# Kernel tuning notes

Measured on AMD Instinct MI355X. Metric: run time of the kernel, lower is better.

## Reference

```python
import jax, jax.numpy as jnp
import numpy as np

EMBED_DIM = 512
EDGE_COUNT = 200
BATCH = 1024
N_SBJ = 1      # subject entities per example
N_OBJ = 64     # candidate object entities per example


def setup_inputs() -> dict:
    key = jax.random.key(0)
    k1, k2, k3, k4 = jax.random.split(key, 4)
    sbj_embs = jax.random.normal(k1, (BATCH, N_SBJ, EMBED_DIM), dtype=jnp.float32)
    obj_embs = jax.random.normal(k2, (BATCH, N_OBJ, EMBED_DIM), dtype=jnp.float32)
    rel_ids = jax.random.randint(k3, (BATCH,), 0, EDGE_COUNT, dtype=jnp.int64)
    # W_r initialized as diagonal matrices from uniform values (as in __init__),
    # but stored as full dense [edge_count, d, d] trainable tensor.
    diag_vals = jax.random.uniform(k4, (EDGE_COUNT, EMBED_DIM), dtype=jnp.float32)
    W_r = jax.vmap(jnp.diag)(diag_vals)  # [edge_count, d, d]
    return {"sbj_embs": sbj_embs, "obj_embs": obj_embs, "rel_ids": rel_ids, "W_r": W_r}


def reference(sbj_embs, obj_embs, rel_ids, W_r):
    # rel_embs: gather per-relation dense matrix  [B, d, d]
    rel_embs = W_r[rel_ids]
    # sbj_rel = sbj @ rel : [B, n, d]
    sbj_rel = jnp.einsum('bnd,bde->bne', sbj_embs, rel_embs)
    # scores = sbj_rel @ obj^T : [B, n, m], then sum over n -> [B, m]
    scores = jnp.einsum('bne,bme->bm', sbj_rel, obj_embs)
    return scores
```

## Files before the change

### kernel.cpp

```cpp
#include <hip/hip_runtime.h>


#define D        512
#define NOBJ     64
#define EDGES    200
#define G        8
#define CSPL     4

__device__ __forceinline__ float4 f4zero() { float4 z; z.x=z.y=z.z=z.w=0.f; return z; }

__global__ __launch_bounds__(256) void prep_kernel(
    const int* __restrict__ rel, int B,
    int* __restrict__ sorted, int* __restrict__ chunk_rel,
    int* __restrict__ chunk_start, int* __restrict__ chunk_cnt,
    int* __restrict__ nchunks)
{
    __shared__ int cnt[EDGES];
    __shared__ int off[EDGES];
    __shared__ int pos[EDGES];
    __shared__ int nch;
    const int t = threadIdx.x;

    if (t < EDGES) cnt[t] = 0;
    if (t == 0) nch = 0;
    __syncthreads();

    for (int b = t; b < B; b += 256) atomicAdd(&cnt[rel[b]], 1);
    __syncthreads();

    if (t == 0) {
        int a = 0;
        for (int r = 0; r < EDGES; ++r) { off[r] = a; a += cnt[r]; }
    }
    if (t < EDGES) pos[t] = 0;
    __syncthreads();

    for (int b = t; b < B; b += 256) {
        const int r = rel[b];
        const int p = atomicAdd(&pos[r], 1);
        sorted[off[r] + p] = b;
    }

    if (t < EDGES) {
        const int n = cnt[t];
        if (n > 0) {
            const int nc   = (n + G - 1) / G;
            const int base = atomicAdd(&nch, nc);
            for (int k = 0; k < nc; ++k) {
                chunk_rel[base + k]   = t;
                chunk_start[base + k] = off[t] + k * G;
                chunk_cnt[base + k]   = min(G, n - k * G);
            }
        }
    }
    __syncthreads();
    if (t == 0) *nchunks = nch;
}

__global__ __launch_bounds__(256) void gemv_kernel(
    const float* __restrict__ sbj, const float* __restrict__ Wr,
    const int* __restrict__ sorted,
    const int* __restrict__ chunk_rel, const int* __restrict__ chunk_start,
    const int* __restrict__ chunk_cnt, const int* __restrict__ nchunks,
    float* __restrict__ V)
{
    const int cid = blockIdx.x >> 2;
    if (cid >= *nchunks) return;
    const int colbase = (blockIdx.x & 3) * 128;
    const int t    = threadIdx.x;
    const int lane = t & 31;
    const int rg   = t >> 5;

    __shared__ float lds[8192];

    const int relid = chunk_rel[cid];
    const int start = chunk_start[cid];
    const int cnt   = chunk_cnt[cid];

    #pragma unroll
    for (int g = 0; g < G; ++g) {
        float2 v2; v2.x = 0.f; v2.y = 0.f;
        if (g < cnt)
            v2 = reinterpret_cast<const float2*>(sbj + (size_t)sorted[start + g] * D)[t];
        lds[g * D + 2 * t]     = v2.x;
        lds[g * D + 2 * t + 1] = v2.y;
    }
    __syncthreads();

    const float4* __restrict__ W4 =
        reinterpret_cast<const float4*>(Wr) + (size_t)relid * (D * D / 4) + (colbase >> 2) + lane;

    float4 acc[G];
    #pragma unroll
    for (int g = 0; g < G; ++g) acc[g] = f4zero();

    #pragma unroll 8
    for (int d8 = 0; d8 < D; d8 += 8) {
        const int row = d8 + rg;
        const float4 w = W4[(size_t)row * (D / 4)];
        #pragma unroll
        for (int g = 0; g < G; ++g) {
            const float sg = lds[g * D + row];
            acc[g].x = fmaf(sg, w.x, acc[g].x);
            acc[g].y = fmaf(sg, w.y, acc[g].y);
            acc[g].z = fmaf(sg, w.z, acc[g].z);
            acc[g].w = fmaf(sg, w.w, acc[g].w);
        }
    }
    __syncthreads();

    #pragma unroll
    for (int g = 0; g < G; ++g)
        reinterpret_cast<float4*>(lds)[(rg * G + g) * 32 + lane] = acc[g];
    __syncthreads();

    const int col = t & 127;
    const int gg  = t >> 7;
    #pragma unroll
    for (int gi = 0; gi < 4; ++gi) {
        const int g = gg * 4 + gi;
        if (g < cnt) {
            float s = 0.f;
            #pragma unroll
            for (int r = 0; r < 8; ++r) s += lds[(r * G + g) * 128 + col];
            V[(size_t)sorted[start + g] * D + colbase + col] = s;
        }
    }
}

__global__ __launch_bounds__(256) void score_kernel(
    const float* __restrict__ V, const float* __restrict__ obj,
    float* __restrict__ out)
{
    const int b    = blockIdx.x;
    const int t    = threadIdx.x;
    const int lane = t & 63;
    const int wv   = t >> 6;

    const float4* __restrict__ v4 = reinterpret_cast<const float4*>(V + (size_t)b * D);
    const float4 a = v4[lane * 2];
    const float4 c = v4[lane * 2 + 1];
    float vreg[8] = {a.x, a.y, a.z, a.w, c.x, c.y, c.z, c.w};

    const float* __restrict__ objb = obj + (size_t)b * NOBJ * D;

    #pragma unroll 4
    for (int j = 0; j < 16; ++j) {
        const int m = wv * 16 + j;
        const float4* __restrict__ o4 = reinterpret_cast<const float4*>(objb + (size_t)m * D);
        const float4 x = o4[lane * 2];
        const float4 y = o4[lane * 2 + 1];

        float p = vreg[0] * x.x + vreg[1] * x.y + vreg[2] * x.z + vreg[3] * x.w
                + vreg[4] * y.x + vreg[5] * y.y + vreg[6] * y.z + vreg[7] * y.w;

        #pragma unroll
        for (int off = 32; off > 0; off >>= 1)
            p += __shfl_down(p, off, 64);

        if (lane == 0) out[(size_t)b * NOBJ + m] = p;
    }
}

__global__ __launch_bounds__(256) void fused_kernel(
    const float* __restrict__ sbj, const float* __restrict__ obj,
    const int* __restrict__ rel, const float* __restrict__ Wr,
    float* __restrict__ out)
{
    const int b = blockIdx.x;
    const int t = threadIdx.x;
    __shared__ float s_lds[D];
    __shared__ float v_lds[D];
    {
        const float2 sv = reinterpret_cast<const float2*>(sbj + (size_t)b * D)[t];
        s_lds[2 * t] = sv.x; s_lds[2 * t + 1] = sv.y;
    }
    __syncthreads();
    const float2* __restrict__ W2 = reinterpret_cast<const float2*>(Wr + (size_t)rel[b] * D * D);
    float acc0 = 0.f, acc1 = 0.f;
    #pragma unroll 8
    for (int d = 0; d < D; ++d) {
        const float sd = s_lds[d];
        const float2 w = W2[d * (D / 2) + t];
        acc0 = fmaf(sd, w.x, acc0); acc1 = fmaf(sd, w.y, acc1);
    }
    v_lds[2 * t] = acc0; v_lds[2 * t + 1] = acc1;
    __syncthreads();
    const int wave = t >> 6, lane = t & 63;
    float vreg[8];
    #pragma unroll
    for (int k = 0; k < 8; ++k) vreg[k] = v_lds[lane * 8 + k];
    const float* __restrict__ objb = obj + (size_t)b * NOBJ * D;
    #pragma unroll 4
    for (int j = 0; j < 16; ++j) {
        const int m = wave * 16 + j;
        const float4* __restrict__ o4 = reinterpret_cast<const float4*>(objb + (size_t)m * D);
        const float4 a = o4[lane * 2];
        const float4 c = o4[lane * 2 + 1];
        float p = vreg[0]*a.x + vreg[1]*a.y + vreg[2]*a.z + vreg[3]*a.w
                + vreg[4]*c.x + vreg[5]*c.y + vreg[6]*c.z + vreg[7]*c.w;
        #pragma unroll
        for (int off = 32; off > 0; off >>= 1) p += __shfl_down(p, off, 64);
        if (lane == 0) out[(size_t)b * NOBJ + m] = p;
    }
}

extern "C" void kernel_launch(void* const* d_in, const int* in_sizes, int n_in,
                              void* d_out, int out_size, void* d_ws, size_t ws_size,
                              hipStream_t stream) {
    const float* sbj = (const float*)d_in[0];
    const float* obj = (const float*)d_in[1];
    const int*   rel = (const int*)d_in[2];
    const float* Wr  = (const float*)d_in[3];
    float*       out = (float*)d_out;
    const int B = in_sizes[2];

    const int maxch = B / G + EDGES;

    const size_t offV      = 0;
    const size_t offSorted = (size_t)B * D * 4;
    const size_t offCRel   = offSorted + (size_t)B * 4;
    const size_t offCStart = offCRel   + (size_t)maxch * 4;
    const size_t offCCnt   = offCStart + (size_t)maxch * 4;
    const size_t offNCh    = offCCnt   + (size_t)maxch * 4;
    const size_t needed    = offNCh + 64;

    if (ws_size < needed) {
        fused_kernel<<<dim3(B), dim3(256), 0, stream>>>(sbj, obj, rel, Wr, out);
        return;
    }

    char* ws = (char*)d_ws;
    float* V           = (float*)(ws + offV);
    int*   sorted      = (int*)(ws + offSorted);
    int*   chunk_rel   = (int*)(ws + offCRel);
    int*   chunk_start = (int*)(ws + offCStart);
    int*   chunk_cnt   = (int*)(ws + offCCnt);
    int*   nchunks     = (int*)(ws + offNCh);

    prep_kernel<<<dim3(1), dim3(256), 0, stream>>>(rel, B, sorted, chunk_rel,
                                                   chunk_start, chunk_cnt, nchunks);
    gemv_kernel<<<dim3(CSPL * maxch), dim3(256), 0, stream>>>(sbj, Wr, sorted,
                                                              chunk_rel, chunk_start,
                                                              chunk_cnt, nchunks, V);
    score_kernel<<<dim3(B), dim3(256), 0, stream>>>(V, obj, out);
}
```

Measured before the change: 375.1 us.

## Fuse score computation into grouped GEMV kernel and parallelize prep scan

Removes the separate score kernel and the intermediate V buffer. Each GEMV block now dots its 128-column slice of the projected subject vector against the matching object columns and accumulates partial scores into the output with atomics. The output is zeroed with a memset first. The single-thread prefix sum in prep is also replaced by a parallel shared-memory scan. This saves the V write and read round trip and one launch, at the cost of four atomic adds per score and an extra memset.

```diff
diff --git a/kernel.cpp b/kernel.cpp
--- a/kernel.cpp
+++ b/kernel.cpp
@@ -15,24 +15,32 @@
     int* __restrict__ chunk_start, int* __restrict__ chunk_cnt,
     int* __restrict__ nchunks)
 {
-    __shared__ int cnt[EDGES];
-    __shared__ int off[EDGES];
-    __shared__ int pos[EDGES];
+    __shared__ int cnt[256];
+    __shared__ int scan[256];
+    __shared__ int off[256];
+    __shared__ int pos[256];
     __shared__ int nch;
     const int t = threadIdx.x;
 
-    if (t < EDGES) cnt[t] = 0;
+    cnt[t] = 0;
+    pos[t] = 0;
     if (t == 0) nch = 0;
     __syncthreads();
 
     for (int b = t; b < B; b += 256) atomicAdd(&cnt[rel[b]], 1);
     __syncthreads();
 
-    if (t == 0) {
-        int a = 0;
-        for (int r = 0; r < EDGES; ++r) { off[r] = a; a += cnt[r]; }
-    }
-    if (t < EDGES) pos[t] = 0;
+    int val = cnt[t];
+    scan[t] = val;
+    __syncthreads();
+    #pragma unroll
+    for (int o = 1; o < 256; o <<= 1) {
+        int v = (t >= o) ? scan[t - o] : 0;
+        __syncthreads();
+        scan[t] += v;
+        __syncthreads();
+    }
+    off[t] = scan[t] - val;
     __syncthreads();
 
     for (int b = t; b < B; b += 256) {
@@ -57,38 +65,45 @@
     if (t == 0) *nchunks = nch;
 }
 
-__global__ __launch_bounds__(256) void gemv_kernel(
-    const float* __restrict__ sbj, const float* __restrict__ Wr,
-    const int* __restrict__ sorted,
+__global__ __launch_bounds__(256) void main_kernel(
+    const float* __restrict__ sbj, const float* __restrict__ obj,
+    const float* __restrict__ Wr,  const int* __restrict__ sorted,
     const int* __restrict__ chunk_rel, const int* __restrict__ chunk_start,
     const int* __restrict__ chunk_cnt, const int* __restrict__ nchunks,
-    float* __restrict__ V)
+    float* __restrict__ out)
 {
     const int cid = blockIdx.x >> 2;
     if (cid >= *nchunks) return;
     const int colbase = (blockIdx.x & 3) * 128;
-    const int t    = threadIdx.x;
-    const int lane = t & 31;
-    const int rg   = t >> 5;
-
-    __shared__ float lds[8192];
+    const int t      = threadIdx.x;
+    const int lane32 = t & 31;
+    const int rg     = t >> 5;
+
+    __shared__ float lds[8192 + 1056];
+    float* s_s   = lds;
+    float* s_par = lds;
+    float* s_vs  = lds + 8192;
 
     const int relid = chunk_rel[cid];
     const int start = chunk_start[cid];
     const int cnt   = chunk_cnt[cid];
 
+    int bidx[G];
+    #pragma unroll
+    for (int g = 0; g < G; ++g) bidx[g] = (g < cnt) ? sorted[start + g] : -1;
+
     #pragma unroll
     for (int g = 0; g < G; ++g) {
         float2 v2; v2.x = 0.f; v2.y = 0.f;
         if (g < cnt)
-            v2 = reinterpret_cast<const float2*>(sbj + (size_t)sorted[start + g] * D)[t];
-        lds[g * D + 2 * t]     = v2.x;
-        lds[g * D + 2 * t + 1] = v2.y;
+            v2 = reinterpret_cast<const float2*>(sbj + (size_t)bidx[g] * D)[t];
+        s_s[g * D + 2 * t]     = v2.x;
+        s_s[g * D + 2 * t + 1] = v2.y;
     }
     __syncthreads();
 
     const float4* __restrict__ W4 =
-        reinterpret_cast<const float4*>(Wr) + (size_t)relid * (D * D / 4) + (colbase >> 2) + lane;
+        reinterpret_cast<const float4*>(Wr) + (size_t)relid * (D * D / 4) + (colbase >> 2) + lane32;
 
     float4 acc[G];
     #pragma unroll
@@ -100,7 +115,7 @@
         const float4 w = W4[(size_t)row * (D / 4)];
         #pragma unroll
         for (int g = 0; g < G; ++g) {
-            const float sg = lds[g * D + row];
+            const float sg = s_s[g * D + row];
             acc[g].x = fmaf(sg, w.x, acc[g].x);
             acc[g].y = fmaf(sg, w.y, acc[g].y);
             acc[g].z = fmaf(sg, w.z, acc[g].z);
@@ -111,54 +126,41 @@
 
     #pragma unroll
     for (int g = 0; g < G; ++g)
-        reinterpret_cast<float4*>(lds)[(rg * G + g) * 32 + lane] = acc[g];
-    __syncthreads();
-
-    const int col = t & 127;
-    const int gg  = t >> 7;
-    #pragma unroll
-    for (int gi = 0; gi < 4; ++gi) {
-        const int g = gg * 4 + gi;
-        if (g < cnt) {
+        reinterpret_cast<float4*>(s_par)[(rg * G + g) * 32 + lane32] = acc[g];
+    __syncthreads();
+
+    {
+        const int col = t & 127;
+        const int gg  = t >> 7;
+        #pragma unroll
+        for (int gi = 0; gi < 4; ++gi) {
+            const int g = gg * 4 + gi;
             float s = 0.f;
             #pragma unroll
-            for (int r = 0; r < 8; ++r) s += lds[(r * G + g) * 128 + col];
-            V[(size_t)sorted[start + g] * D + colbase + col] = s;
-        }
-    }
-}
-
-__global__ __launch_bounds__(256) void score_kernel(
-    const float* __restrict__ V, const float* __restrict__ obj,
-    float* __restrict__ out)
-{
-    const int b    = blockIdx.x;
-    const int t    = threadIdx.x;
-    const int lane = t & 63;
-    const int wv   = t >> 6;
-
-    const float4* __restrict__ v4 = reinterpret_cast<const float4*>(V + (size_t)b * D);
-    const float4 a = v4[lane * 2];
-    const float4 c = v4[lane * 2 + 1];
-    float vreg[8] = {a.x, a.y, a.z, a.w, c.x, c.y, c.z, c.w};
-
-    const float* __restrict__ objb = obj + (size_t)b * NOBJ * D;
-
-    #pragma unroll 4
-    for (int j = 0; j < 16; ++j) {
-        const int m = wv * 16 + j;
-        const float4* __restrict__ o4 = reinterpret_cast<const float4*>(objb + (size_t)m * D);
-        const float4 x = o4[lane * 2];
-        const float4 y = o4[lane * 2 + 1];
-
-        float p = vreg[0] * x.x + vreg[1] * x.y + vreg[2] * x.z + vreg[3] * x.w
-                + vreg[4] * y.x + vreg[5] * y.y + vreg[6] * y.z + vreg[7] * y.w;
-
-        #pragma unroll
-        for (int off = 32; off > 0; off >>= 1)
-            p += __shfl_down(p, off, 64);
-
-        if (lane == 0) out[(size_t)b * NOBJ + m] = p;
+            for (int r = 0; r < 8; ++r) s += s_par[(r * G + g) * 128 + col];
+            s_vs[g * 132 + (col >> 5) * 33 + (col & 31)] = s;
+        }
+    }
+    __syncthreads();
+
+    const int pair = t & 3;
+    const int m    = t >> 2;
+
+    for (int g = 0; g < cnt; ++g) {
+        const float* __restrict__ op =
+            obj + (size_t)bidx[g] * NOBJ * D + (size_t)m * D + colbase + pair * 32;
+        const float* __restrict__ vp = s_vs + g * 132 + pair * 33;
+
+        float p = 0.f;
+        #pragma unroll
+        for (int j = 0; j < 8; ++j) {
+            const float4 o = reinterpret_cast<const float4*>(op)[j];
+            p += vp[4 * j]     * o.x + vp[4 * j + 1] * o.y
+               + vp[4 * j + 2] * o.z + vp[4 * j + 3] * o.w;
+        }
+        p += __shfl_xor(p, 1);
+        p += __shfl_xor(p, 2);
+        if (pair == 0) atomicAdd(&out[(size_t)bidx[g] * NOBJ + m], p);
     }
 }
 
@@ -193,15 +195,15 @@
     const float* __restrict__ objb = obj + (size_t)b * NOBJ * D;
     #pragma unroll 4
     for (int j = 0; j < 16; ++j) {
-        const int m = wave * 16 + j;
-        const float4* __restrict__ o4 = reinterpret_cast<const float4*>(objb + (size_t)m * D);
+        const int mm = wave * 16 + j;
+        const float4* __restrict__ o4 = reinterpret_cast<const float4*>(objb + (size_t)mm * D);
         const float4 a = o4[lane * 2];
         const float4 c = o4[lane * 2 + 1];
         float p = vreg[0]*a.x + vreg[1]*a.y + vreg[2]*a.z + vreg[3]*a.w
                 + vreg[4]*c.x + vreg[5]*c.y + vreg[6]*c.z + vreg[7]*c.w;
         #pragma unroll
         for (int off = 32; off > 0; off >>= 1) p += __shfl_down(p, off, 64);
-        if (lane == 0) out[(size_t)b * NOBJ + m] = p;
+        if (lane == 0) out[(size_t)b * NOBJ + mm] = p;
     }
 }
 
@@ -217,8 +219,7 @@
 
     const int maxch = B / G + EDGES;
 
-    const size_t offV      = 0;
-    const size_t offSorted = (size_t)B * D * 4;
+    const size_t offSorted = 0;
     const size_t offCRel   = offSorted + (size_t)B * 4;
     const size_t offCStart = offCRel   + (size_t)maxch * 4;
     const size_t offCCnt   = offCStart + (size_t)maxch * 4;
@@ -231,17 +232,17 @@
     }
 
     char* ws = (char*)d_ws;
-    float* V           = (float*)(ws + offV);
-    int*   sorted      = (int*)(ws + offSorted);
-    int*   chunk_rel   = (int*)(ws + offCRel);
-    int*   chunk_start = (int*)(ws + offCStart);
-    int*   chunk_cnt   = (int*)(ws + offCCnt);
-    int*   nchunks     = (int*)(ws + offNCh);
+    int* sorted      = (int*)(ws + offSorted);
+    int* chunk_rel   = (int*)(ws + offCRel);
+    int* chunk_start = (int*)(ws + offCStart);
+    int* chunk_cnt   = (int*)(ws + offCCnt);
+    int* nchunks     = (int*)(ws + offNCh);
+
+    hipMemsetAsync(out, 0, (size_t)out_size * sizeof(float), stream);
 
     prep_kernel<<<dim3(1), dim3(256), 0, stream>>>(rel, B, sorted, chunk_rel,
                                                    chunk_start, chunk_cnt, nchunks);
-    gemv_kernel<<<dim3(CSPL * maxch), dim3(256), 0, stream>>>(sbj, Wr, sorted,
+    main_kernel<<<dim3(CSPL * maxch), dim3(256), 0, stream>>>(sbj, obj, Wr, sorted,
                                                               chunk_rel, chunk_start,
-                                                              chunk_cnt, nchunks, V);
-    score_kernel<<<dim3(B), dim3(256), 0, stream>>>(V, obj, out);
-}
+                                                              chunk_cnt, nchunks, out);
+}
```

Measured after the change: 389.8 us. +3.9%, slower.
